# Performance work log

Hardware: AMD Instinct MI355X
Metric: run time of the kernel (lower is better)

The kernel has to match this reference:

```python
import jax, jax.numpy as jnp
import numpy as np


def setup_inputs() -> dict:
    key = jax.random.key(0)
    ks = jax.random.split(key, 5)
    B, S, H, I = 8, 2048, 1024, 4096
    # int8 quantized activation / weights / int8 bias, held as int32 for portability
    hidden_states = jax.random.randint(ks[0], (B, S, H), -128, 128, dtype=jnp.int32)
    w_fc = jax.random.randint(ks[1], (H, I), -128, 128, dtype=jnp.int32)   # Conv1D weight [in, out]
    b_fc = jax.random.randint(ks[2], (I,), -128, 128, dtype=jnp.int32)     # int8 bias (B8)
    w_proj = jax.random.randint(ks[3], (I, H), -128, 128, dtype=jnp.int32)
    b_proj = jax.random.normal(ks[4], (H,), dtype=jnp.float32)             # fp32 bias (BFP32)
    alpha_fc = jnp.float32(0.004)   # (x_scale * w_scale / out_scale) of c_fc
    beta_fc = jnp.float32(0.02)     # bias_scale / out_scale of c_fc
    alpha_proj = jnp.float32(0.003) # x_scale * w_scale of c_proj (dequant to fp32)
    return {
        "hidden_states": hidden_states,
        "w_fc": w_fc, "b_fc": b_fc, "alpha_fc": alpha_fc, "beta_fc": beta_fc,
        "w_proj": w_proj, "b_proj": b_proj, "alpha_proj": alpha_proj,
    }


def reference(hidden_states, w_fc, b_fc, alpha_fc, beta_fc, w_proj, b_proj, alpha_proj):
    # ---- c_fc: W8A8B8O8 Conv1D + fused ReLU + requantization to int8 ----
    acc1 = jnp.matmul(hidden_states, w_fc)                       # [B,S,I] int32
    h = acc1.astype(jnp.float32) * alpha_fc + b_fc.astype(jnp.float32) * beta_fc
    h = jax.nn.relu(h)
    # requantize to int8 (round + saturate)
    h_q = jnp.clip(jnp.round(h), -128.0, 127.0).astype(jnp.int32)  # [B,S,I]
    # ---- c_proj: W8A8BFP32OFP32 Conv1D (dequant to fp32) ----
    acc2 = jnp.matmul(h_q, w_proj)                               # [B,S,H] int32
    out = acc2.astype(jnp.float32) * alpha_proj + b_proj
    # dropout is identity in eval mode
    return out
```

## Files before the change

kernel.cpp:

```cpp
#include <hip/hip_runtime.h>
#include <cstdint>
#include <cstddef>

typedef int int4v __attribute__((ext_vector_type(4)));
typedef signed char schar;

#define DEVI __device__ __forceinline__

DEVI void load_lds16(const void* g, void* l) {
  __builtin_amdgcn_global_load_lds(
      (const __attribute__((address_space(1))) void*)g,
      (__attribute__((address_space(3))) void*)l, 16, 0, 0);
}

#define BAR() __builtin_amdgcn_s_barrier()
#define LGKM(n) asm volatile("s_waitcnt lgkmcnt(" #n ")")
#define VMW(n) asm volatile("s_waitcnt vmcnt(" #n ")")

__global__ __launch_bounds__(256) void pack_i8(const int* __restrict__ src,
                                               signed char* __restrict__ dst,
                                               int n4) {
  int i = blockIdx.x * 256 + threadIdx.x;
  if (i >= n4) return;
  int4v v = ((const int4v*)src)[i];
  int p = (v.x & 255) | ((v.y & 255) << 8) | ((v.z & 255) << 16) | (v.w << 24);
  ((int*)dst)[i] = p;
}

__global__ __launch_bounds__(256) void pack_wT(const int* __restrict__ w,
                                               signed char* __restrict__ wT,
                                               int K, int N) {
  __shared__ signed char t[64][68];
  int n0 = blockIdx.x * 64, k0 = blockIdx.y * 64;
  int tr = threadIdx.x >> 6, tc = threadIdx.x & 63;
#pragma unroll
  for (int i = 0; i < 16; ++i) {
    int r = i * 4 + tr;
    t[r][tc] = (signed char)w[(size_t)(k0 + r) * N + n0 + tc];
  }
  __syncthreads();
#pragma unroll
  for (int i = 0; i < 16; ++i) {
    int r = i * 4 + tr;
    wT[(size_t)(n0 + r) * K + k0 + tc] = t[tc][r];
  }
}

template <int EPI>
__global__ __launch_bounds__(1024, 4) void gemmC(
    const schar* __restrict__ A, const schar* __restrict__ BT,
    int M, int N, int K, const int* __restrict__ bias_i,
    const float* __restrict__ alphaP, const float* __restrict__ betaP,
    const float* __restrict__ bias_f, schar* __restrict__ outQ,
    float* __restrict__ outF) {
  extern __shared__ schar lds[];

  const int tid = threadIdx.x;
  const int wid = tid >> 6, lane = tid & 63;
  const int wr = wid >> 2, wc = wid & 3;
  const int l16 = lane & 15, l4 = lane >> 4;

  const int gx = gridDim.x;
  const int nwg = gx * gridDim.y;
  const int bid = blockIdx.y * gx + blockIdx.x;
  const int swz = (bid & 7) * (nwg >> 3) + (bid >> 3);
  const int rowBase = (swz / gx) * 256;
  const int colBase = (swz % gx) * 256;
  const int NT = K >> 7;

  const float alpha = alphaP[0];
  const float beta = (EPI == 0) ? betaP[0] : 0.f;
  asm volatile("" ::"s"(alpha), "s"(beta));
  LGKM(0);

  const schar* gA[2];
  const schar* gB[2];
#pragma unroll
  for (int c = 0; c < 2; ++c) {
    int o = c * 16384 + tid * 16;
    int r = o >> 7;
    int g = ((o >> 4) & 7) ^ (r & 7);
    gA[c] = A + (size_t)(rowBase + r) * K + g * 16;
    gB[c] = BT + (size_t)(colBase + r) * K + g * 16;
  }
  auto stage = [&](int buf, int t) {
    schar* dA = lds + buf * 32768 + wid * 1024;
    schar* dB = lds + 65536 + buf * 32768 + wid * 1024;
    load_lds16(gA[0] + (size_t)t * 128, dA);
    load_lds16(gA[1] + (size_t)t * 128, dA + 16384);
    load_lds16(gB[0] + (size_t)t * 128, dB);
    load_lds16(gB[1] + (size_t)t * 128, dB + 16384);
  };

  const int so0 = ((0 + l4) ^ (l16 & 7)) * 16 + l16 * 128;
  const int so1 = ((4 + l4) ^ (l16 & 7)) * 16 + l16 * 128;
  const int sA = (wid & 1) ? so1 : so0;
  const int sB = (wid & 1) ? so0 : so1;
  const int aoff = wr * 8192;
  const int boff = wc * 8192;

  int4v acc[4][4] = {};
  int4v aF[4], bF[4];

#define RDALL(SO, Ab, Bb)                                         \
  do {                                                            \
    aF[0] = *(const int4v*)((Ab) + aoff + 0 * 2048 + (SO));       \
    _Pragma("unroll") for (int ni = 0; ni < 4; ++ni) bF[ni] =     \
        *(const int4v*)((Bb) + boff + ni * 2048 + (SO));          \
    _Pragma("unroll") for (int mi = 1; mi < 4; ++mi) aF[mi] =     \
        *(const int4v*)((Ab) + aoff + mi * 2048 + (SO));          \
  } while (0)
#define MMALL()                                                        \
  do {                                                                 \
    __builtin_amdgcn_s_setprio(1);                                     \
    _Pragma("unroll") for (int mi = 0; mi < 4; ++mi)                   \
        _Pragma("unroll") for (int ni = 0; ni < 4; ++ni) acc[mi][ni] = \
        __builtin_amdgcn_mfma_i32_16x16x64_i8(aF[mi], bF[ni],          \
                                              acc[mi][ni], 0, 0, 0);   \
    __builtin_amdgcn_s_setprio(0);                                     \
  } while (0)

  stage(0, 0);
  VMW(0);
  BAR();

  for (int T = 0; T < NT; ++T) {
    const int cb = T & 1;
    const schar* Ab = lds + cb * 32768;
    const schar* Bb = lds + 65536 + cb * 32768;

    if (T + 1 < NT) stage(cb ^ 1, T + 1);

    RDALL(sA, Ab, Bb);
    MMALL();
    RDALL(sB, Ab, Bb);
    MMALL();

    LGKM(0);
    VMW(0);
    BAR();
  }

  if (EPI == 0) {
#pragma unroll
    for (int MI = 0; MI < 4; ++MI) {
      int row = rowBase + wr * 64 + MI * 16 + l4 * 4;
#pragma unroll
      for (int NI = 0; NI < 4; ++NI) {
        int col = colBase + wc * 64 + NI * 16 + l16;
        float bt = (float)bias_i[col] * beta;
#pragma unroll
        for (int j = 0; j < 4; ++j) {
          float h = (float)acc[MI][NI][j] * alpha + bt;
          h = fmaxf(h, 0.f);
          h = rintf(h);
          h = fminf(h, 127.f);
          outQ[(size_t)(row + j) * N + col] = (schar)h;
        }
      }
    }
  } else {
#pragma unroll
    for (int MI = 0; MI < 4; ++MI) {
      int row = rowBase + wr * 64 + MI * 16 + l4 * 4;
#pragma unroll
      for (int NI = 0; NI < 4; ++NI) {
        int col = colBase + wc * 64 + NI * 16 + l16;
        float bv = bias_f[col];
#pragma unroll
        for (int j = 0; j < 4; ++j)
          outF[(size_t)(row + j) * N + col] =
              (float)acc[MI][NI][j] * alpha + bv;
      }
    }
  }
#undef RDALL
#undef MMALL
}

extern "C" void kernel_launch(void* const* d_in, const int* in_sizes, int n_in,
                              void* d_out, int out_size, void* d_ws,
                              size_t ws_size, hipStream_t stream) {
  const int M = 16384, H = 1024, I = 4096;
  const int* hidden = (const int*)d_in[0];
  const int* w_fc = (const int*)d_in[1];
  const int* b_fc = (const int*)d_in[2];
  const float* alpha_fc = (const float*)d_in[3];
  const float* beta_fc = (const float*)d_in[4];
  const int* w_proj = (const int*)d_in[5];
  const float* b_proj = (const float*)d_in[6];
  const float* alpha_proj = (const float*)d_in[7];
  float* out = (float*)d_out;

  signed char* hq = (signed char*)d_ws;
  signed char* aP = hq + (size_t)M * I;
  signed char* wfcT = aP + (size_t)M * H;
  signed char* wpT = wfcT + (size_t)I * H;

  hipFuncSetAttribute((const void*)gemmC<0>,
                      hipFuncAttributeMaxDynamicSharedMemorySize, 131072);
  hipFuncSetAttribute((const void*)gemmC<1>,
                      hipFuncAttributeMaxDynamicSharedMemorySize, 131072);

  pack_i8<<<(M * H / 4 + 255) / 256, 256, 0, stream>>>(hidden, aP, M * H / 4);
  pack_wT<<<dim3(I / 64, H / 64), 256, 0, stream>>>(w_fc, wfcT, H, I);
  pack_wT<<<dim3(H / 64, I / 64), 256, 0, stream>>>(w_proj, wpT, I, H);

  gemmC<0><<<dim3(I / 256, M / 256), 1024, 131072, stream>>>(
      aP, wfcT, M, I, H, b_fc, alpha_fc, beta_fc, nullptr, hq, nullptr);
  gemmC<1><<<dim3(H / 256, M / 256), 1024, 131072, stream>>>(
      hq, wpT, M, H, I, nullptr, alpha_proj, nullptr, b_proj, nullptr, out);
}
```

Measured before the change: 173.7 us.

## Switch GEMM to 64-wide K tiles with four-stage LDS ring buffer

The int8 GEMM now stages 64-wide K slices instead of 128-wide ones. It keeps four LDS slots, each holding A and B for one slice, in place of two double-buffered 128-K stages, and uses a new XOR swizzle matched to the 64-byte rows. Each loop iteration issues prefetches two slices ahead and runs two MFMA groups, with one barrier per pair of slices. The intent is deeper prefetch to better hide global-load latency at the same LDS footprint, at the cost of a changed bank-swizzle pattern and more, smaller load instructions.

```diff
diff --git a/kernel.cpp b/kernel.cpp
--- a/kernel.cpp
+++ b/kernel.cpp
@@ -47,7 +47,7 @@
 }
 
 template <int EPI>
-__global__ __launch_bounds__(1024, 4) void gemmC(
+__global__ __launch_bounds__(1024, 4) void gemmV(
     const schar* __restrict__ A, const schar* __restrict__ BT,
     int M, int N, int K, const int* __restrict__ bias_i,
     const float* __restrict__ alphaP, const float* __restrict__ betaP,
@@ -66,51 +66,40 @@
   const int swz = (bid & 7) * (nwg >> 3) + (bid >> 3);
   const int rowBase = (swz / gx) * 256;
   const int colBase = (swz % gx) * 256;
-  const int NT = K >> 7;
+  const int NT = K >> 6;
 
   const float alpha = alphaP[0];
   const float beta = (EPI == 0) ? betaP[0] : 0.f;
   asm volatile("" ::"s"(alpha), "s"(beta));
   LGKM(0);
 
-  const schar* gA[2];
-  const schar* gB[2];
-#pragma unroll
-  for (int c = 0; c < 2; ++c) {
-    int o = c * 16384 + tid * 16;
-    int r = o >> 7;
-    int g = ((o >> 4) & 7) ^ (r & 7);
-    gA[c] = A + (size_t)(rowBase + r) * K + g * 16;
-    gB[c] = BT + (size_t)(colBase + r) * K + g * 16;
-  }
+  const int o = tid * 16;
+  const int rr = o >> 6;
+  const int gsl = ((o >> 4) & 3) ^ ((rr >> 1) & 3);
+  const schar* gAs = A + (size_t)(rowBase + rr) * K + gsl * 16;
+  const schar* gBs = BT + (size_t)(colBase + rr) * K + gsl * 16;
+
   auto stage = [&](int buf, int t) {
-    schar* dA = lds + buf * 32768 + wid * 1024;
-    schar* dB = lds + 65536 + buf * 32768 + wid * 1024;
-    load_lds16(gA[0] + (size_t)t * 128, dA);
-    load_lds16(gA[1] + (size_t)t * 128, dA + 16384);
-    load_lds16(gB[0] + (size_t)t * 128, dB);
-    load_lds16(gB[1] + (size_t)t * 128, dB + 16384);
+    schar* d = lds + buf * 32768 + wid * 1024;
+    load_lds16(gAs + (size_t)t * 64, d);
+    load_lds16(gBs + (size_t)t * 64, d + 16384);
   };
 
-  const int so0 = ((0 + l4) ^ (l16 & 7)) * 16 + l16 * 128;
-  const int so1 = ((4 + l4) ^ (l16 & 7)) * 16 + l16 * 128;
-  const int sA = (wid & 1) ? so1 : so0;
-  const int sB = (wid & 1) ? so0 : so1;
-  const int aoff = wr * 8192;
-  const int boff = wc * 8192;
+  const int slotc = (l4 ^ ((l16 >> 1) & 3)) * 16 + l16 * 64;
+  const int aoff = wr * 4096 + slotc;
+  const int boff = 16384 + wc * 4096 + slotc;
 
   int4v acc[4][4] = {};
   int4v aF[4], bF[4];
 
-#define RDALL(SO, Ab, Bb)                                         \
-  do {                                                            \
-    aF[0] = *(const int4v*)((Ab) + aoff + 0 * 2048 + (SO));       \
-    _Pragma("unroll") for (int ni = 0; ni < 4; ++ni) bF[ni] =     \
-        *(const int4v*)((Bb) + boff + ni * 2048 + (SO));          \
-    _Pragma("unroll") for (int mi = 1; mi < 4; ++mi) aF[mi] =     \
-        *(const int4v*)((Ab) + aoff + mi * 2048 + (SO));          \
+#define RDT(Bu)                                                    \
+  do {                                                             \
+    _Pragma("unroll") for (int mi = 0; mi < 4; ++mi) aF[mi] =      \
+        *(const int4v*)((Bu) + aoff + mi * 1024);                  \
+    _Pragma("unroll") for (int ni = 0; ni < 4; ++ni) bF[ni] =      \
+        *(const int4v*)((Bu) + boff + ni * 1024);                  \
   } while (0)
-#define MMALL()                                                        \
+#define MMT()                                                          \
   do {                                                                 \
     __builtin_amdgcn_s_setprio(1);                                     \
     _Pragma("unroll") for (int mi = 0; mi < 4; ++mi)                   \
@@ -121,20 +110,18 @@
   } while (0)
 
   stage(0, 0);
+  stage(1, 1);
   VMW(0);
   BAR();
 
-  for (int T = 0; T < NT; ++T) {
-    const int cb = T & 1;
-    const schar* Ab = lds + cb * 32768;
-    const schar* Bb = lds + 65536 + cb * 32768;
-
-    if (T + 1 < NT) stage(cb ^ 1, T + 1);
-
-    RDALL(sA, Ab, Bb);
-    MMALL();
-    RDALL(sB, Ab, Bb);
-    MMALL();
+  for (int T = 0; T < NT; T += 2) {
+    if (T + 2 < NT) stage((T + 2) & 3, T + 2);
+    if (T + 3 < NT) stage((T + 3) & 3, T + 3);
+
+    RDT(lds + (T & 3) * 32768);
+    MMT();
+    RDT(lds + ((T + 1) & 3) * 32768);
+    MMT();
 
     LGKM(0);
     VMW(0);
@@ -174,8 +161,8 @@
       }
     }
   }
-#undef RDALL
-#undef MMALL
+#undef RDT
+#undef MMT
 }
 
 extern "C" void kernel_launch(void* const* d_in, const int* in_sizes, int n_in,
@@ -197,17 +184,17 @@
   signed char* wfcT = aP + (size_t)M * H;
   signed char* wpT = wfcT + (size_t)I * H;
 
-  hipFuncSetAttribute((const void*)gemmC<0>,
+  hipFuncSetAttribute((const void*)gemmV<0>,
                       hipFuncAttributeMaxDynamicSharedMemorySize, 131072);
-  hipFuncSetAttribute((const void*)gemmC<1>,
+  hipFuncSetAttribute((const void*)gemmV<1>,
                       hipFuncAttributeMaxDynamicSharedMemorySize, 131072);
 
   pack_i8<<<(M * H / 4 + 255) / 256, 256, 0, stream>>>(hidden, aP, M * H / 4);
   pack_wT<<<dim3(I / 64, H / 64), 256, 0, stream>>>(w_fc, wfcT, H, I);
   pack_wT<<<dim3(H / 64, I / 64), 256, 0, stream>>>(w_proj, wpT, I, H);
 
-  gemmC<0><<<dim3(I / 256, M / 256), 1024, 131072, stream>>>(
+  gemmV<0><<<dim3(I / 256, M / 256), 1024, 131072, stream>>>(
       aP, wfcT, M, I, H, b_fc, alpha_fc, beta_fc, nullptr, hq, nullptr);
-  gemmC<1><<<dim3(H / 256, M / 256), 1024, 131072, stream>>>(
+  gemmV<1><<<dim3(H / 256, M / 256), 1024, 131072, stream>>>(
       hq, wpT, M, H, I, nullptr, alpha_proj, nullptr, b_proj, nullptr, out);
 }
```

Measured after the change: 177.6 us. 1.02x slower.
